# Optimization experiments

Measured on AMD Instinct MI355X. Metric: run time of the kernel, lower is better.

The kernel has to match this reference:

```python
import jax, jax.numpy as jnp
import numpy as np

N = 100000      # nodes
E = 1000000     # edges per branch
C_IN = 128      # in_channels
C_OUT = 64      # out_channels
BN_EPS = 1e-5


def setup_inputs() -> dict:
    key = jax.random.key(0)
    ks = jax.random.split(key, 8)
    inp = {"x": jax.random.normal(ks[0], (N, C_IN), jnp.float32)}
    for i, name in enumerate(["edge_index_p", "edge_index_s", "edge_index_v"]):
        inp[name] = jax.random.randint(ks[1 + i], (2, E), 0, N, dtype=jnp.int32)
    # input BatchNorm1d affine params
    inp["in_gamma"] = jnp.ones((C_IN,), jnp.float32)
    inp["in_beta"] = jnp.zeros((C_IN,), jnp.float32)
    # per-branch GIN MLP params, stacked over the 3 branches (p, s, v)
    inp["W1"] = jax.random.normal(ks[4], (3, C_IN, C_OUT), jnp.float32) * 0.05
    inp["b1"] = jnp.zeros((3, C_OUT), jnp.float32)
    inp["W2"] = jax.random.normal(ks[5], (3, C_OUT, C_OUT), jnp.float32) * 0.05
    inp["b2"] = jnp.zeros((3, C_OUT), jnp.float32)
    # per-branch output BatchNorm1d affine params
    inp["bn_gamma"] = jnp.ones((3, C_OUT), jnp.float32)
    inp["bn_beta"] = jnp.zeros((3, C_OUT), jnp.float32)
    return inp


def _batchnorm(h, gamma, beta):
    # training-mode BatchNorm1d: batch stats over the node dim, biased variance
    mu = h.mean(axis=0)
    var = ((h - mu) ** 2).mean(axis=0)
    return gamma * (h - mu) * jax.lax.rsqrt(var + BN_EPS) + beta


def reference(x, edge_index_p, edge_index_s, edge_index_v,
              in_gamma, in_beta, W1, b1, W2, b2, bn_gamma, bn_beta):
    n = x.shape[0]
    xn = _batchnorm(x, in_gamma, in_beta)  # in_norm
    outs = []
    for i, ei in enumerate([edge_index_p, edge_index_s, edge_index_v]):
        src, dst = ei[0], ei[1]
        # GINConv (eps=0): sum-aggregate neighbor features, add self
        agg = jax.ops.segment_sum(xn[src], dst, num_segments=n)  # [N, C_IN]
        h = xn + agg
        # MLP([C_IN, C_OUT, C_OUT]) with ReLU between, plain last layer
        h = jax.nn.relu(h @ W1[i] + b1[i])
        h = h @ W2[i] + b2[i]
        # post-GIN BatchNorm1d + Tanh
        outs.append(jnp.tanh(_batchnorm(h, bn_gamma[i], bn_beta[i])))
    return tuple(outs)  # (x_p, x_s, x_v)
```

## Files before the change

kernel.cpp:

```cpp
#include <hip/hip_runtime.h>
#include <math.h>

#define NN   100000
#define NE   1000000
#define CIN  128
#define COUT 64
#define BN_EPS 1e-5f
#define NB    391
#define NBLK1 128
#define CHUNK_E ((NE + NBLK1 - 1) / NBLK1)
#define NT    32
#define NTILE (NN / NT)

#define Y1B_OFF    0
#define COL_OFF    9600000
#define ROWPTR_OFF 12600000
#define OFF_OFF    12900016
#define W1P_OFF    13050160
#define C1_OFF     (W1P_OFF + 3*CIN*COUT)
#define INSUM_OFF  (C1_OFF + 3*COUT)
#define INSQ_OFF   (INSUM_OFF + CIN)
#define OSUM_OFF   (INSQ_OFF + CIN)
#define OSQ_OFF    (OSUM_OFF + 3*COUT)
#define SCALE_OFF  (OSQ_OFF + 3*COUT)
#define SHIFT_OFF  (SCALE_OFF + CIN)
#define OBNS_OFF   (SHIFT_OFF + CIN)
#define OBNB_OFF   (OBNS_OFF + 3*COUT)
#define ZERO_OFF   INSUM_OFF
#define ZERO_CNT   (2*CIN + 6*COUT)

__device__ __forceinline__ unsigned bf16_rne(float f) {
    unsigned u = __float_as_uint(f);
    return (u + 0x7FFFu + ((u >> 16) & 1u)) >> 16;
}
__device__ __forceinline__ float lo16f(unsigned u) { return __uint_as_float(u << 16); }
__device__ __forceinline__ float hi16f(unsigned u) { return __uint_as_float(u & 0xFFFF0000u); }

__global__ __launch_bounds__(256) void k_in_stats(const float* __restrict__ x,
                                                  float* __restrict__ ws) {
    int tid = blockIdx.x * blockDim.x + threadIdx.x;
    int c = tid & (CIN - 1);
    int r0 = tid >> 7;
    int rstride = (gridDim.x * blockDim.x) >> 7;
    float s = 0.f, ss = 0.f;
    for (int r = r0; r < NN; r += rstride) {
        float v = x[(size_t)r * CIN + c];
        s += v; ss += v * v;
    }
    unsafeAtomicAdd(&ws[INSUM_OFF + c], s);
    unsafeAtomicAdd(&ws[INSQ_OFF + c], ss);
}

__global__ void k_in_finalize(const float* __restrict__ g, const float* __restrict__ b,
                              float* __restrict__ ws) {
    int c = threadIdx.x;
    float mu  = ws[INSUM_OFF + c] * (1.f / NN);
    float var = ws[INSQ_OFF + c] * (1.f / NN) - mu * mu;
    float sc  = g[c] * rsqrtf(var + BN_EPS);
    ws[SCALE_OFF + c] = sc;
    ws[SHIFT_OFF + c] = b[c] - mu * sc;
}

__global__ void k_fold(const float* __restrict__ W1, float* __restrict__ ws) {
    int idx = blockIdx.x * blockDim.x + threadIdx.x;
    int k = (idx >> 6) & (CIN - 1);
    ws[W1P_OFF + idx] = ws[SCALE_OFF + k] * W1[idx];
}

__global__ void k_c1(const float* __restrict__ W1, float* __restrict__ ws) {
    int i = blockIdx.x, o = threadIdx.x;
    float acc = 0.f;
    for (int k = 0; k < CIN; ++k)
        acc = fmaf(ws[SHIFT_OFF + k], W1[i * CIN * COUT + k * COUT + o], acc);
    ws[C1_OFF + i * COUT + o] = acc;
}

__global__ __launch_bounds__(256) void k_sort_hist(const int* __restrict__ e0,
                                                   const int* __restrict__ e1,
                                                   const int* __restrict__ e2,
                                                   int* __restrict__ wsi) {
    int z = blockIdx.y;
    const int* ei = (z == 0) ? e0 : (z == 1) ? e1 : e2;
    __shared__ int h[NB];
    for (int i = threadIdx.x; i < NB; i += 256) h[i] = 0;
    __syncthreads();
    int beg = blockIdx.x * CHUNK_E;
    int end = min(NE, beg + CHUNK_E);
    for (int e = beg + threadIdx.x; e < end; e += 256)
        atomicAdd(&h[ei[NE + e] >> 8], 1);
    __syncthreads();
    int* off = wsi + OFF_OFF + z * (NB * NBLK1);
    for (int i = threadIdx.x; i < NB; i += 256)
        off[i * NBLK1 + blockIdx.x] = h[i];
}

__global__ __launch_bounds__(1024) void k_sort_scan(int* __restrict__ wsi) {
    int z = blockIdx.x;
    int* off = wsi + OFF_OFF + z * (NB * NBLK1);
    const int TOT = NB * NBLK1;
    const int CH = (TOT + 1023) / 1024;
    __shared__ int sh[1024];
    int t = threadIdx.x;
    int base = t * CH;
    int s = 0;
    for (int i = 0; i < CH; ++i) {
        int idx = base + i;
        if (idx < TOT) s += off[idx];
    }
    sh[t] = s;
    __syncthreads();
    for (int o = 1; o < 1024; o <<= 1) {
        int v = (t >= o) ? sh[t - o] : 0;
        __syncthreads();
        sh[t] += v;
        __syncthreads();
    }
    int run = sh[t] - s;
    for (int i = 0; i < CH; ++i) {
        int idx = base + i;
        if (idx < TOT) {
            int v = off[idx];
            off[idx] = run;
            run += v;
        }
    }
}

__global__ __launch_bounds__(256) void k_sort_scatter(const int* __restrict__ e0,
                                                      const int* __restrict__ e1,
                                                      const int* __restrict__ e2,
                                                      int* __restrict__ wsi) {
    int z = blockIdx.y;
    const int* ei = (z == 0) ? e0 : (z == 1) ? e1 : e2;
    const int* off = wsi + OFF_OFF + z * (NB * NBLK1);
    int2* temp = (int2*)wsi + (size_t)z * NE;
    __shared__ int cur[NB];
    for (int i = threadIdx.x; i < NB; i += 256)
        cur[i] = off[i * NBLK1 + blockIdx.x];
    __syncthreads();
    int beg = blockIdx.x * CHUNK_E;
    int end = min(NE, beg + CHUNK_E);
    for (int e = beg + threadIdx.x; e < end; e += 256) {
        int d = ei[NE + e];
        int s = ei[e];
        int pos = atomicAdd(&cur[d >> 8], 1);
        temp[pos] = make_int2(d, s);
    }
}

__global__ __launch_bounds__(256) void k_bucket(int* __restrict__ wsi) {
    int z = blockIdx.y, bk = blockIdx.x;
    const int* off = wsi + OFF_OFF + z * (NB * NBLK1);
    const int2* temp = (const int2*)wsi + (size_t)z * NE;
    int* col    = wsi + COL_OFF + z * NE;
    int* rowptr = wsi + ROWPTR_OFF + z * (NN + 1);
    int bs = off[bk * NBLK1];
    int be = (bk + 1 < NB) ? off[(bk + 1) * NBLK1] : NE;
    __shared__ int h[256], sc[256], cur[256];
    int t = threadIdx.x;
    h[t] = 0;
    __syncthreads();
    for (int e = bs + t; e < be; e += 256)
        atomicAdd(&h[temp[e].x & 255], 1);
    __syncthreads();
    int v = h[t];
    sc[t] = v;
    __syncthreads();
    for (int o = 1; o < 256; o <<= 1) {
        int u = (t >= o) ? sc[t - o] : 0;
        __syncthreads();
        sc[t] += u;
        __syncthreads();
    }
    int excl = sc[t] - v;
    int gd = bk * 256 + t;
    if (gd <= NN) rowptr[gd] = bs + excl;
    cur[t] = excl;
    __syncthreads();
    for (int e = bs + t; e < be; e += 256) {
        int2 p = temp[e];
        int pos = atomicAdd(&cur[p.x & 255], 1);
        col[bs + pos] = p.y;
    }
}

__global__ __launch_bounds__(256, 2) void k_gemm1(const float* __restrict__ x,
                                                  const float* __restrict__ W1p_all,
                                                  const float* __restrict__ c1_all,
                                                  unsigned* __restrict__ y1b_all) {
    int lane = threadIdx.x & 63;
    int wave = (blockIdx.x * blockDim.x + threadIdx.x) >> 6;
    int nw   = (gridDim.x * blockDim.x) >> 6;
    float c1v0 = c1_all[lane];
    float c1v1 = c1_all[COUT + lane];
    float c1v2 = c1_all[2 * COUT + lane];
    const int NGRP = NN / 8;
    for (int g = wave; g < NGRP; g += nw) {
        int n0 = __builtin_amdgcn_readfirstlane(g) * 8;
        const float* __restrict__ xr = x + (size_t)n0 * CIN;
        float a0[8], a1[8], a2[8];
        #pragma unroll
        for (int i = 0; i < 8; ++i) { a0[i] = c1v0; a1[i] = c1v1; a2[i] = c1v2; }
        #pragma unroll 1
        for (int kc = 0; kc < CIN; kc += 16) {
            float w0[16], w1[16], w2[16];
            #pragma unroll
            for (int j = 0; j < 16; ++j) {
                w0[j] = W1p_all[(kc + j) * COUT + lane];
                w1[j] = W1p_all[CIN * COUT + (kc + j) * COUT + lane];
                w2[j] = W1p_all[2 * CIN * COUT + (kc + j) * COUT + lane];
            }
            #pragma unroll
            for (int i = 0; i < 8; ++i) {
                #pragma unroll
                for (int j = 0; j < 16; ++j) {
                    float xv = xr[i * CIN + kc + j];
                    a0[i] = fmaf(xv, w0[j], a0[i]);
                    a1[i] = fmaf(xv, w1[j], a1[i]);
                    a2[i] = fmaf(xv, w2[j], a2[i]);
                }
            }
        }
        #define STORE_NODE(zz, az, i) { \
            float vhi_ = __shfl(az[i], (lane & 31) + 32); \
            if (lane < 32) { \
                unsigned wrd_ = bf16_rne(az[i]) | (bf16_rne(vhi_) << 16); \
                y1b_all[((size_t)(zz) * NN + n0 + (i)) * 32 + lane] = wrd_; \
            } }
        #pragma unroll
        for (int i = 0; i < 8; ++i) {
            STORE_NODE(0, a0, i)
            STORE_NODE(1, a1, i)
            STORE_NODE(2, a2, i)
        }
        #undef STORE_NODE
    }
}

__global__ __launch_bounds__(256) void k_gather(const float* __restrict__ b1all,
                                                float* __restrict__ tall,
                                                float* __restrict__ ws) {
    int z = blockIdx.y;
    const unsigned* __restrict__ y1b = (const unsigned*)ws + Y1B_OFF + (size_t)z * NN * 32;
    float* __restrict__ t = tall + (size_t)z * NN * COUT;
    const int* __restrict__ rowptr = (const int*)ws + ROWPTR_OFF + z * (NN + 1);
    const int* __restrict__ col    = (const int*)ws + COL_OFF + z * NE;
    int lane = threadIdx.x & 63;
    int w32  = lane & 31;
    int half = lane >> 5;
    float b1lo = b1all[z * COUT + w32];
    float b1hi = b1all[z * COUT + 32 + w32];
    int wave = (blockIdx.x * blockDim.x + threadIdx.x) >> 6;
    int nw   = (gridDim.x * blockDim.x) >> 6;
    const int NP = NN / 2;
    for (int p = wave; p < NP; p += nw) {
        int n = p * 2 + half;
        int beg = rowptr[n], end = rowptr[n + 1];
        unsigned su = y1b[(size_t)n * 32 + w32];
        float alo = lo16f(su), ahi = hi16f(su);
        float blo = 0.f, bhi = 0.f, clo = 0.f, chi = 0.f, dlo = 0.f, dhi = 0.f;
        int j = beg;
        for (; j + 3 < end; j += 4) {
            int c0 = col[j], c1 = col[j + 1], c2 = col[j + 2], c3 = col[j + 3];
            unsigned u0 = y1b[(size_t)c0 * 32 + w32];
            unsigned u1 = y1b[(size_t)c1 * 32 + w32];
            unsigned u2 = y1b[(size_t)c2 * 32 + w32];
            unsigned u3 = y1b[(size_t)c3 * 32 + w32];
            alo += lo16f(u0); ahi += hi16f(u0);
            blo += lo16f(u1); bhi += hi16f(u1);
            clo += lo16f(u2); chi += hi16f(u2);
            dlo += lo16f(u3); dhi += hi16f(u3);
        }
        for (; j < end; ++j) {
            unsigned u = y1b[(size_t)col[j] * 32 + w32];
            alo += lo16f(u); ahi += hi16f(u);
        }
        t[(size_t)n * 64 + w32]      = fmaxf((alo + blo) + (clo + dlo) + b1lo, 0.f);
        t[(size_t)n * 64 + 32 + w32] = fmaxf((ahi + bhi) + (chi + dhi) + b1hi, 0.f);
    }
}

__global__ __launch_bounds__(256) void k_mlp2(const float* __restrict__ W2all,
                                              const float* __restrict__ b2all,
                                              float* __restrict__ outall,
                                              float* __restrict__ ws) {
    int z = blockIdx.y;
    __shared__ float w2s[COUT * COUT];
    __shared__ float ts[NT][COUT];
    const float* __restrict__ W2 = W2all + z * COUT * COUT;
    float* __restrict__ out = outall + (size_t)z * NN * COUT;
    int tid = threadIdx.x;
    for (int i = tid; i < COUT * COUT; i += 256) w2s[i] = W2[i];
    int lane = tid & 63;
    int wave = tid >> 6;
    int n0 = wave * 8;
    float b2v = b2all[z * COUT + lane];
    float ls = 0.f, lss = 0.f;
    for (int tile = blockIdx.x; tile < NTILE; tile += gridDim.x) {
        __syncthreads();
        {
            const float4* __restrict__ src =
                (const float4*)(out + (size_t)tile * NT * COUT);
            float4* dst = (float4*)ts;
            dst[tid] = src[tid];
            dst[tid + 256] = src[tid + 256];
        }
        __syncthreads();
        float a0 = b2v, a1 = b2v, a2 = b2v, a3 = b2v;
        float a4 = b2v, a5 = b2v, a6 = b2v, a7 = b2v;
        #pragma unroll
        for (int jq = 0; jq < 16; ++jq) {
            float wj0 = w2s[(4 * jq)     * COUT + lane];
            float wj1 = w2s[(4 * jq + 1) * COUT + lane];
            float wj2 = w2s[(4 * jq + 2) * COUT + lane];
            float wj3 = w2s[(4 * jq + 3) * COUT + lane];
            float4 t0 = *(const float4*)&ts[n0 + 0][4 * jq];
            float4 t1 = *(const float4*)&ts[n0 + 1][4 * jq];
            float4 t2 = *(const float4*)&ts[n0 + 2][4 * jq];
            float4 t3 = *(const float4*)&ts[n0 + 3][4 * jq];
            float4 t4 = *(const float4*)&ts[n0 + 4][4 * jq];
            float4 t5 = *(const float4*)&ts[n0 + 5][4 * jq];
            float4 t6 = *(const float4*)&ts[n0 + 6][4 * jq];
            float4 t7 = *(const float4*)&ts[n0 + 7][4 * jq];
            a0 = fmaf(t0.x, wj0, a0); a0 = fmaf(t0.y, wj1, a0);
            a0 = fmaf(t0.z, wj2, a0); a0 = fmaf(t0.w, wj3, a0);
            a1 = fmaf(t1.x, wj0, a1); a1 = fmaf(t1.y, wj1, a1);
            a1 = fmaf(t1.z, wj2, a1); a1 = fmaf(t1.w, wj3, a1);
            a2 = fmaf(t2.x, wj0, a2); a2 = fmaf(t2.y, wj1, a2);
            a2 = fmaf(t2.z, wj2, a2); a2 = fmaf(t2.w, wj3, a2);
            a3 = fmaf(t3.x, wj0, a3); a3 = fmaf(t3.y, wj1, a3);
            a3 = fmaf(t3.z, wj2, a3); a3 = fmaf(t3.w, wj3, a3);
            a4 = fmaf(t4.x, wj0, a4); a4 = fmaf(t4.y, wj1, a4);
            a4 = fmaf(t4.z, wj2, a4); a4 = fmaf(t4.w, wj3, a4);
            a5 = fmaf(t5.x, wj0, a5); a5 = fmaf(t5.y, wj1, a5);
            a5 = fmaf(t5.z, wj2, a5); a5 = fmaf(t5.w, wj3, a5);
            a6 = fmaf(t6.x, wj0, a6); a6 = fmaf(t6.y, wj1, a6);
            a6 = fmaf(t6.z, wj2, a6); a6 = fmaf(t6.w, wj3, a6);
            a7 = fmaf(t7.x, wj0, a7); a7 = fmaf(t7.y, wj1, a7);
            a7 = fmaf(t7.z, wj2, a7); a7 = fmaf(t7.w, wj3, a7);
        }
        size_t base = (size_t)tile * NT * COUT + (size_t)n0 * COUT;
        out[base + lane] = a0;
        out[base + COUT + lane] = a1;
        out[base + 2 * COUT + lane] = a2;
        out[base + 3 * COUT + lane] = a3;
        out[base + 4 * COUT + lane] = a4;
        out[base + 5 * COUT + lane] = a5;
        out[base + 6 * COUT + lane] = a6;
        out[base + 7 * COUT + lane] = a7;
        ls += ((a0 + a1) + (a2 + a3)) + ((a4 + a5) + (a6 + a7));
        lss += ((a0 * a0 + a1 * a1) + (a2 * a2 + a3 * a3))
             + ((a4 * a4 + a5 * a5) + (a6 * a6 + a7 * a7));
    }
    unsafeAtomicAdd(&ws[OSUM_OFF + z * COUT + lane], ls);
    unsafeAtomicAdd(&ws[OSQ_OFF + z * COUT + lane], lss);
}

__global__ void k_obn_final(const float* __restrict__ g, const float* __restrict__ b,
                            float* __restrict__ ws) {
    int br = blockIdx.x;
    int o = threadIdx.x;
    float mu  = ws[OSUM_OFF + br * COUT + o] * (1.f / NN);
    float var = ws[OSQ_OFF  + br * COUT + o] * (1.f / NN) - mu * mu;
    float sc  = g[br * COUT + o] * rsqrtf(var + BN_EPS);
    ws[OBNS_OFF + br * COUT + o] = sc;
    ws[OBNB_OFF + br * COUT + o] = b[br * COUT + o] - mu * sc;
}

__global__ __launch_bounds__(256) void k_apply(float* __restrict__ outall,
                                               const float* __restrict__ ws) {
    int z = blockIdx.y;
    float* out = outall + (size_t)z * NN * COUT;
    const float* __restrict__ sc = ws + OBNS_OFF + z * COUT;
    const float* __restrict__ sh = ws + OBNB_OFF + z * COUT;
    int idx = blockIdx.x * blockDim.x + threadIdx.x;
    int stride = gridDim.x * blockDim.x;
    const int total = NN * COUT / 4;
    float4* o4 = (float4*)out;
    for (int v = idx; v < total; v += stride) {
        int c = (v & 15) * 4;
        float4 f = o4[v];
        f.x = tanhf(fmaf(f.x, sc[c],     sh[c]));
        f.y = tanhf(fmaf(f.y, sc[c + 1], sh[c + 1]));
        f.z = tanhf(fmaf(f.z, sc[c + 2], sh[c + 2]));
        f.w = tanhf(fmaf(f.w, sc[c + 3], sh[c + 3]));
        o4[v] = f;
    }
}

extern "C" void kernel_launch(void* const* d_in, const int* in_sizes, int n_in,
                              void* d_out, int out_size, void* d_ws, size_t ws_size,
                              hipStream_t stream) {
    const float* x   = (const float*)d_in[0];
    const int*   eip = (const int*)d_in[1];
    const int*   eis = (const int*)d_in[2];
    const int*   eiv = (const int*)d_in[3];
    const float* ig  = (const float*)d_in[4];
    const float* ib  = (const float*)d_in[5];
    const float* W1  = (const float*)d_in[6];
    const float* b1  = (const float*)d_in[7];
    const float* W2  = (const float*)d_in[8];
    const float* b2  = (const float*)d_in[9];
    const float* bng = (const float*)d_in[10];
    const float* bnb = (const float*)d_in[11];
    float* out = (float*)d_out;
    float* ws  = (float*)d_ws;
    int*   wsi = (int*)d_ws;

    hipMemsetAsync(ws + ZERO_OFF, 0, ZERO_CNT * sizeof(float), stream);

    k_in_stats<<<256, 256, 0, stream>>>(x, ws);
    k_in_finalize<<<1, 128, 0, stream>>>(ig, ib, ws);
    k_fold<<<96, 256, 0, stream>>>(W1, ws);
    k_c1<<<3, 64, 0, stream>>>(W1, ws);

    k_sort_hist<<<dim3(NBLK1, 3), 256, 0, stream>>>(eip, eis, eiv, wsi);
    k_sort_scan<<<3, 1024, 0, stream>>>(wsi);
    k_sort_scatter<<<dim3(NBLK1, 3), 256, 0, stream>>>(eip, eis, eiv, wsi);
    k_bucket<<<dim3(NB, 3), 256, 0, stream>>>(wsi);

    k_gemm1<<<1024, 256, 0, stream>>>(x, ws + W1P_OFF, ws + C1_OFF,
                                      (unsigned*)ws + Y1B_OFF);
    k_gather<<<dim3(2048, 3), 256, 0, stream>>>(b1, out, ws);
    k_mlp2<<<dim3(512, 3), 256, 0, stream>>>(W2, b2, out, ws);
    k_obn_final<<<3, 64, 0, stream>>>(bng, bnb, ws);
    k_apply<<<dim3(1024, 3), 256, 0, stream>>>(out, ws);
}
```

Before: 546.4 us.

## Fuse neighbor gather with second MLP layer into one kernel via shared tile

Merges the CSR gather/ReLU kernel into the second-layer GEMM kernel. Each block gathers its 32-node tile's aggregated first-layer activations straight into shared memory and then runs the 64x64 matmul, so the intermediate no longer takes a global write and re-read, and one launch is dropped. The cost is that the fused kernel runs 512x3 blocks rather than 2048x3 for the latency-bound gather, with __syncthreads between the gather and GEMM phases, which may reduce memory-level parallelism for the irregular loads.

```diff
diff --git a/kernel.cpp b/kernel.cpp
--- a/kernel.cpp
+++ b/kernel.cpp
@@ -237,73 +237,57 @@
     }
 }
 
-__global__ __launch_bounds__(256) void k_gather(const float* __restrict__ b1all,
-                                                float* __restrict__ tall,
-                                                float* __restrict__ ws) {
-    int z = blockIdx.y;
-    const unsigned* __restrict__ y1b = (const unsigned*)ws + Y1B_OFF + (size_t)z * NN * 32;
-    float* __restrict__ t = tall + (size_t)z * NN * COUT;
-    const int* __restrict__ rowptr = (const int*)ws + ROWPTR_OFF + z * (NN + 1);
-    const int* __restrict__ col    = (const int*)ws + COL_OFF + z * NE;
-    int lane = threadIdx.x & 63;
-    int w32  = lane & 31;
-    int half = lane >> 5;
-    float b1lo = b1all[z * COUT + w32];
-    float b1hi = b1all[z * COUT + 32 + w32];
-    int wave = (blockIdx.x * blockDim.x + threadIdx.x) >> 6;
-    int nw   = (gridDim.x * blockDim.x) >> 6;
-    const int NP = NN / 2;
-    for (int p = wave; p < NP; p += nw) {
-        int n = p * 2 + half;
-        int beg = rowptr[n], end = rowptr[n + 1];
-        unsigned su = y1b[(size_t)n * 32 + w32];
-        float alo = lo16f(su), ahi = hi16f(su);
-        float blo = 0.f, bhi = 0.f, clo = 0.f, chi = 0.f, dlo = 0.f, dhi = 0.f;
-        int j = beg;
-        for (; j + 3 < end; j += 4) {
-            int c0 = col[j], c1 = col[j + 1], c2 = col[j + 2], c3 = col[j + 3];
-            unsigned u0 = y1b[(size_t)c0 * 32 + w32];
-            unsigned u1 = y1b[(size_t)c1 * 32 + w32];
-            unsigned u2 = y1b[(size_t)c2 * 32 + w32];
-            unsigned u3 = y1b[(size_t)c3 * 32 + w32];
-            alo += lo16f(u0); ahi += hi16f(u0);
-            blo += lo16f(u1); bhi += hi16f(u1);
-            clo += lo16f(u2); chi += hi16f(u2);
-            dlo += lo16f(u3); dhi += hi16f(u3);
-        }
-        for (; j < end; ++j) {
-            unsigned u = y1b[(size_t)col[j] * 32 + w32];
-            alo += lo16f(u); ahi += hi16f(u);
-        }
-        t[(size_t)n * 64 + w32]      = fmaxf((alo + blo) + (clo + dlo) + b1lo, 0.f);
-        t[(size_t)n * 64 + 32 + w32] = fmaxf((ahi + bhi) + (chi + dhi) + b1hi, 0.f);
-    }
-}
-
-__global__ __launch_bounds__(256) void k_mlp2(const float* __restrict__ W2all,
-                                              const float* __restrict__ b2all,
-                                              float* __restrict__ outall,
-                                              float* __restrict__ ws) {
+__global__ __launch_bounds__(256) void k_gm(const float* __restrict__ b1all,
+                                            const float* __restrict__ W2all,
+                                            const float* __restrict__ b2all,
+                                            float* __restrict__ outall,
+                                            float* __restrict__ ws) {
     int z = blockIdx.y;
     __shared__ float w2s[COUT * COUT];
     __shared__ float ts[NT][COUT];
-    const float* __restrict__ W2 = W2all + z * COUT * COUT;
+    const unsigned* __restrict__ y1b = (const unsigned*)ws + Y1B_OFF + (size_t)z * NN * 32;
+    const int* __restrict__ rowptr = (const int*)ws + ROWPTR_OFF + z * (NN + 1);
+    const int* __restrict__ col    = (const int*)ws + COL_OFF + z * NE;
     float* __restrict__ out = outall + (size_t)z * NN * COUT;
     int tid = threadIdx.x;
-    for (int i = tid; i < COUT * COUT; i += 256) w2s[i] = W2[i];
+    for (int i = tid; i < COUT * COUT; i += 256) w2s[i] = W2all[z * COUT * COUT + i];
     int lane = tid & 63;
+    int w32  = lane & 31;
+    int hw   = tid >> 5;
     int wave = tid >> 6;
     int n0 = wave * 8;
-    float b2v = b2all[z * COUT + lane];
+    float b1lo = b1all[z * COUT + w32];
+    float b1hi = b1all[z * COUT + 32 + w32];
+    float b2v  = b2all[z * COUT + lane];
     float ls = 0.f, lss = 0.f;
     for (int tile = blockIdx.x; tile < NTILE; tile += gridDim.x) {
         __syncthreads();
-        {
-            const float4* __restrict__ src =
-                (const float4*)(out + (size_t)tile * NT * COUT);
-            float4* dst = (float4*)ts;
-            dst[tid] = src[tid];
-            dst[tid + 256] = src[tid + 256];
+        #pragma unroll 1
+        for (int q = 0; q < 4; ++q) {
+            int nn = hw + q * 8;
+            int n = tile * NT + nn;
+            int beg = rowptr[n], end = rowptr[n + 1];
+            unsigned su = y1b[(size_t)n * 32 + w32];
+            float alo = lo16f(su), ahi = hi16f(su);
+            float blo = 0.f, bhi = 0.f, clo = 0.f, chi = 0.f, dlo = 0.f, dhi = 0.f;
+            int j = beg;
+            for (; j + 3 < end; j += 4) {
+                int c0 = col[j], c1 = col[j + 1], c2 = col[j + 2], c3 = col[j + 3];
+                unsigned u0 = y1b[(size_t)c0 * 32 + w32];
+                unsigned u1 = y1b[(size_t)c1 * 32 + w32];
+                unsigned u2 = y1b[(size_t)c2 * 32 + w32];
+                unsigned u3 = y1b[(size_t)c3 * 32 + w32];
+                alo += lo16f(u0); ahi += hi16f(u0);
+                blo += lo16f(u1); bhi += hi16f(u1);
+                clo += lo16f(u2); chi += hi16f(u2);
+                dlo += lo16f(u3); dhi += hi16f(u3);
+            }
+            for (; j < end; ++j) {
+                unsigned u = y1b[(size_t)col[j] * 32 + w32];
+                alo += lo16f(u); ahi += hi16f(u);
+            }
+            ts[nn][w32]      = fmaxf((alo + blo) + (clo + dlo) + b1lo, 0.f);
+            ts[nn][32 + w32] = fmaxf((ahi + bhi) + (chi + dhi) + b1hi, 0.f);
         }
         __syncthreads();
         float a0 = b2v, a1 = b2v, a2 = b2v, a3 = b2v;
@@ -421,8 +405,7 @@
 
     k_gemm1<<<1024, 256, 0, stream>>>(x, ws + W1P_OFF, ws + C1_OFF,
                                       (unsigned*)ws + Y1B_OFF);
-    k_gather<<<dim3(2048, 3), 256, 0, stream>>>(b1, out, ws);
-    k_mlp2<<<dim3(512, 3), 256, 0, stream>>>(W2, b2, out, ws);
+    k_gm<<<dim3(512, 3), 256, 0, stream>>>(b1, W2, b2, out, ws);
     k_obn_final<<<3, 64, 0, stream>>>(bng, bnb, ws);
     k_apply<<<dim3(1024, 3), 256, 0, stream>>>(out, ws);
 }
```

New measurement: 602.5 us. +10.3%, slower.
